# Kernel optimization log

Measured on AMD Instinct MI355X. Metric: run time of the kernel, lower is better.

## Reference

```python
import jax, jax.numpy as jnp
import numpy as np

B, T, N, M = 128, 64, 128, 256


def setup_inputs() -> dict:
    key = jax.random.key(0)
    ks = jax.random.split(key, 8)
    s = 0.05  # small init scale to avoid tanh/sigmoid saturation
    return {
        "data": jax.random.normal(ks[0], (B, T, N), jnp.float32),
        "h0": jnp.zeros((B, M), jnp.float32),
        "c0": jnp.zeros((B, M), jnp.float32),
        "W": jax.random.normal(ks[1], (N, 4 * M), jnp.float32) * s,   # LSTM kernel (i,f,c,o)
        "U": jax.random.normal(ks[2], (M, 4 * M), jnp.float32) * s,   # LSTM recurrent kernel
        "b": jnp.zeros((4 * M,), jnp.float32),
        "w1_k": jax.random.normal(ks[3], (T, T), jnp.float32) * s,
        "w1_b": jnp.zeros((T,), jnp.float32),
        "w2_k": jax.random.normal(ks[4], (2 * M, T), jnp.float32) * s,
        "w2_b": jnp.zeros((T,), jnp.float32),
        "v_k": jax.random.normal(ks[5], (T, 1), jnp.float32) * s,
        "v_b": jnp.zeros((1,), jnp.float32),
        "n": N,
    }


def reference(data, h0, c0, W, U, b, w1_k, w1_b, w2_k, w2_b, v_k, v_b, n):
    Tn = data.shape[1]
    # w1 applied to x_perm = (B, n, T); constant across timesteps -> precompute
    w1x = jnp.einsum('btf,ts->bfs', data, w1_k) + w1_b  # (B, n, T)

    def step(carry, x_t):
        h, c = carry
        # keras LSTM cell, gate order i, f, c(g), o
        z = x_t @ W + h @ U + b                      # (B, 4m)
        i, f, g, o = jnp.split(z, 4, axis=-1)
        i = jax.nn.sigmoid(i)
        f = jax.nn.sigmoid(f)
        g = jnp.tanh(g)
        o = jax.nn.sigmoid(o)
        c2 = f * c + i * g
        h2 = o * jnp.tanh(c2)
        # input attention, computed with post-step (h2, c2) as in the original
        q = jnp.concatenate([h2, c2], axis=-1) @ w2_k + w2_b   # (B, T)
        score = jnp.tanh(w1x + q[:, None, :])                  # (B, n, T)
        s = score @ v_k[:, 0] + v_b[0]                         # (B, n)
        alpha = jax.nn.softmax(s, axis=-1)                     # softmax over features n
        return (h2, c2), alpha

    xs = jnp.swapaxes(data, 0, 1)                    # (T, B, n)
    _, alphas = jax.lax.scan(step, (h0, c0), xs)     # (T, B, n)
    # faithful to tf.reshape(stack(T,B,1,n), (-1, T, n)) in the original
    alpha_seq = alphas.reshape(-1, Tn, n)            # (B, T, n)
    return data * alpha_seq
```

## Files before the change

kernel.cpp:

```cpp
#include <hip/hip_runtime.h>

typedef unsigned short u16;
typedef __attribute__((ext_vector_type(8))) short short8;
typedef __attribute__((ext_vector_type(4))) float f32x4;

#define DEVI static __device__ __forceinline__

DEVI u16 f2bf(float f) {
  union { float f; unsigned u; } v; v.f = f;
  unsigned r = v.u + 0x7FFFu + ((v.u >> 16) & 1u);
  return (u16)(r >> 16);
}

DEVI float bf2f(u16 x) {
  union { unsigned u; float f; } v; v.u = ((unsigned)x) << 16;
  return v.f;
}

DEVI short8 pack8(float4 a, float4 b) {
  short8 v;
  v[0] = (short)f2bf(a.x); v[1] = (short)f2bf(a.y);
  v[2] = (short)f2bf(a.z); v[3] = (short)f2bf(a.w);
  v[4] = (short)f2bf(b.x); v[5] = (short)f2bf(b.y);
  v[6] = (short)f2bf(b.z); v[7] = (short)f2bf(b.w);
  return v;
}

DEVI float sigm(float x) {
  return __builtin_amdgcn_rcpf(1.f + __expf(-x));
}
DEVI float tanh_(float x) {
  return 1.f - 2.f * __builtin_amdgcn_rcpf(__expf(2.f * x) + 1.f);
}

__global__ __launch_bounds__(256) void k_prep(
    const float* __restrict__ W, const float* __restrict__ U,
    const float* __restrict__ w2k, u16* __restrict__ Wt,
    u16* __restrict__ Ut, u16* __restrict__ w2t) {
  int idx = blockIdx.x * 256 + threadIdx.x;
  int stride = gridDim.x * 256;
  for (int i = idx; i < 256 * 1024; i += stride) {
    int k = i >> 10, j = i & 1023;
    Ut[j * 256 + k] = f2bf(U[i]);
  }
  for (int i = idx; i < 128 * 1024; i += stride) {
    int k = i >> 10, j = i & 1023;
    Wt[j * 128 + k] = f2bf(W[i]);
  }
  for (int i = idx; i < 512 * 64; i += stride) {
    int k = i >> 6, s = i & 63;
    w2t[s * 512 + k] = f2bf(w2k[i]);
  }
}

__global__ __launch_bounds__(512) void k_xw(
    const float* __restrict__ data, const float* __restrict__ bias,
    const u16* __restrict__ Wt, u16* __restrict__ XWf) {
  __shared__ u16 Xs[16][136];
  const int tid = threadIdx.x;
  const int lane = tid & 63;
  const int w = tid >> 6;
  const int l15 = lane & 15;
  const int l4 = lane >> 4;
  const int t = blockIdx.x >> 3, bg = blockIdx.x & 7, b0 = bg << 4;

  if (tid < 256) {
    int row = tid >> 4, cb = (tid & 15) * 8;
    const float4* p = reinterpret_cast<const float4*>(
        &data[(size_t)(b0 + row) * 8192 + t * 128 + cb]);
    float4 va = p[0], vb = p[1];
    *reinterpret_cast<short8*>(&Xs[row][cb]) = pack8(va, vb);
  }
  __syncthreads();

  f32x4 acc[8];
#pragma unroll
  for (int ct = 0; ct < 8; ++ct) {
    float bv = bias[w * 128 + ct * 16 + l15];
    acc[ct] = (f32x4){bv, bv, bv, bv};
  }
#pragma unroll
  for (int kk = 0; kk < 4; ++kk) {
    short8 af = *reinterpret_cast<const short8*>(&Xs[l15][kk * 32 + l4 * 8]);
#pragma unroll
    for (int ct = 0; ct < 8; ++ct) {
      const int col = w * 128 + ct * 16 + l15;
      short8 bf =
          *reinterpret_cast<const short8*>(&Wt[col * 128 + kk * 32 + l4 * 8]);
      acc[ct] = __builtin_amdgcn_mfma_f32_16x16x32_bf16(af, bf, acc[ct], 0, 0, 0);
    }
  }
#pragma unroll
  for (int ct = 0; ct < 8; ++ct) {
    const int ft = w * 8 + ct;
    ushort4 v;
    v.x = f2bf(acc[ct][0]); v.y = f2bf(acc[ct][1]);
    v.z = f2bf(acc[ct][2]); v.w = f2bf(acc[ct][3]);
    *reinterpret_cast<ushort4*>(
        &XWf[((size_t)(t * 8 + bg) * 64 + ft) * 256 + lane * 4]) = v;
  }
}

__global__ __launch_bounds__(512, 2) void k_lstm(
    const float* __restrict__ h0, const float* __restrict__ c0,
    const float* __restrict__ w2b, const u16* __restrict__ Ut,
    const u16* __restrict__ w2t, const u16* __restrict__ XWf,
    float* __restrict__ QS) {
  __shared__ u16 Hs[2][16][264];
  __shared__ u16 Cs[2][16][264];

  const int tid = threadIdx.x;
  const int lane = tid & 63;
  const int w = tid >> 6;
  const int l15 = lane & 15;
  const int l4 = lane >> 4;
  const int bg = blockIdx.x;
  const int b0 = bg << 4;

  {
    int row = tid >> 5, hb = (tid & 31) * 8;
    const float4* p =
        reinterpret_cast<const float4*>(&h0[(size_t)(b0 + row) * 256 + hb]);
    float4 a0 = p[0], a1 = p[1];
    *reinterpret_cast<short8*>(&Hs[0][row][hb]) = pack8(a0, a1);
  }

  float creg[2][4];
#pragma unroll
  for (int n = 0; n < 2; ++n)
#pragma unroll
    for (int r = 0; r < 4; ++r)
      creg[n][r] = c0[(size_t)(b0 + l4 * 4 + r) * 256 + w * 32 + n * 16 + l15];

  float w2bv = (w < 4) ? w2b[w * 16 + l15] : 0.f;

  __syncthreads();

  for (int t = 0; t < 64; ++t) {
    const int cur = t & 1, nxt = cur ^ 1;

    f32x4 acc[4][2];
#pragma unroll
    for (int g = 0; g < 4; ++g)
#pragma unroll
      for (int n = 0; n < 2; ++n) {
        const int ft = g * 16 + w * 2 + n;
        ushort4 v = *reinterpret_cast<const ushort4*>(
            &XWf[((size_t)(t * 8 + bg) * 64 + ft) * 256 + lane * 4]);
        acc[g][n] = (f32x4){bf2f(v.x), bf2f(v.y), bf2f(v.z), bf2f(v.w)};
      }

#pragma unroll
    for (int kk = 0; kk < 8; ++kk) {
      short8 af =
          *reinterpret_cast<const short8*>(&Hs[cur][l15][kk * 32 + l4 * 8]);
#pragma unroll
      for (int g = 0; g < 4; ++g)
#pragma unroll
        for (int n = 0; n < 2; ++n) {
          const int col = g * 256 + w * 32 + n * 16 + l15;
          short8 bf = *reinterpret_cast<const short8*>(
              &Ut[(size_t)col * 256 + kk * 32 + l4 * 8]);
          acc[g][n] =
              __builtin_amdgcn_mfma_f32_16x16x32_bf16(af, bf, acc[g][n], 0, 0, 0);
        }
    }

#pragma unroll
    for (int n = 0; n < 2; ++n)
#pragma unroll
      for (int r = 0; r < 4; ++r) {
        float iv = sigm(acc[0][n][r]);
        float fv = sigm(acc[1][n][r]);
        float gv = tanh_(acc[2][n][r]);
        float ov = sigm(acc[3][n][r]);
        float c2 = fv * creg[n][r] + iv * gv;
        creg[n][r] = c2;
        float h2 = ov * tanh_(c2);
        int m = w * 32 + n * 16 + l15;
        int br = l4 * 4 + r;
        Hs[nxt][br][m] = f2bf(h2);
        Cs[nxt][br][m] = f2bf(c2);
      }
    __syncthreads();

    if (w < 4) {
      f32x4 qa = (f32x4){w2bv, w2bv, w2bv, w2bv};
      const int colq = w * 16 + l15;
#pragma unroll
      for (int kk = 0; kk < 16; ++kk) {
        short8 af;
        if (kk < 8)
          af = *reinterpret_cast<const short8*>(
              &Hs[nxt][l15][kk * 32 + l4 * 8]);
        else
          af = *reinterpret_cast<const short8*>(
              &Cs[nxt][l15][(kk - 8) * 32 + l4 * 8]);
        short8 bf = *reinterpret_cast<const short8*>(
            &w2t[colq * 512 + kk * 32 + l4 * 8]);
        qa = __builtin_amdgcn_mfma_f32_16x16x32_bf16(af, bf, qa, 0, 0, 0);
      }
#pragma unroll
      for (int r = 0; r < 4; ++r)
        QS[(size_t)(t * 128 + b0 + l4 * 4 + r) * 64 + w * 16 + l15] = qa[r];
    }
  }
}

__global__ __launch_bounds__(256) void k_attn(
    const float* __restrict__ data, const float* __restrict__ w1k,
    const float* __restrict__ w1b, const float* __restrict__ vk,
    const float* __restrict__ vb, const float* __restrict__ QS,
    float* __restrict__ out) {
  __shared__ float Xs[64][128];
  __shared__ float Wk[64][64];
  __shared__ float w1x[128][67];
  __shared__ float vls[64];
  __shared__ float qls[2][64];
  __shared__ float red[4][2];

  const int tid = threadIdx.x;
  const int b = blockIdx.x >> 1;
  const int half = blockIdx.x & 1;

#pragma unroll
  for (int c = 0; c < 8; ++c) {
    int i = c * 1024 + tid * 4;
    *reinterpret_cast<float4*>(&Xs[0][0] + i) =
        *reinterpret_cast<const float4*>(&data[(size_t)b * 8192 + i]);
  }
#pragma unroll
  for (int c = 0; c < 4; ++c) {
    int i = c * 1024 + tid * 4;
    *reinterpret_cast<float4*>(&Wk[0][0] + i) =
        *reinterpret_cast<const float4*>(&w1k[i]);
  }
  if (tid < 64) vls[tid] = vk[tid];
  __syncthreads();

  const int f = tid & 127;
  const int sh = tid >> 7;
  const int s0 = sh * 32;
  {
    float a[32];
#pragma unroll
    for (int j = 0; j < 32; ++j) a[j] = w1b[s0 + j];
    for (int t = 0; t < 64; ++t) {
      float xv = Xs[t][f];
#pragma unroll
      for (int j = 0; j < 32; ++j) a[j] = __fmaf_rn(xv, Wk[t][s0 + j], a[j]);
    }
#pragma unroll
    for (int j = 0; j < 32; ++j) w1x[f][s0 + j] = a[j];
  }
  __syncthreads();

  const float vbv = vb[0];
  const int wv = tid >> 6;
  const int lane = tid & 63;

  for (int tt = 0; tt < 16; ++tt) {
    if (tid < 128) {
      int which = tid >> 6, s = tid & 63;
      qls[which][s] =
          QS[(size_t)((half * 32 + tt * 2 + which) * 128 + b) * 64 + s];
    }
    __syncthreads();

    float acc = vbv;
#pragma unroll 8
    for (int s = 0; s < 64; ++s)
      acc += tanh_(w1x[f][s] + qls[sh][s]) * vls[s];

    float m = acc;
#pragma unroll
    for (int o = 32; o > 0; o >>= 1) m = fmaxf(m, __shfl_xor(m, o));
    if (lane == 0) red[wv][0] = m;
    __syncthreads();
    m = fmaxf(red[sh * 2][0], red[sh * 2 + 1][0]);
    float e = __expf(acc - m);
    float sum = e;
#pragma unroll
    for (int o = 32; o > 0; o >>= 1) sum += __shfl_xor(sum, o);
    if (lane == 0) red[wv][1] = sum;
    __syncthreads();
    sum = red[sh * 2][1] + red[sh * 2 + 1][1];
    float alpha = e / sum;

    int t = half * 32 + tt * 2 + sh;
    size_t P = (size_t)t * 128 + b;
    out[P * 128 + f] = data[P * 128 + f] * alpha;
    __syncthreads();
  }
}

extern "C" void kernel_launch(void* const* d_in, const int* in_sizes, int n_in,
                              void* d_out, int out_size, void* d_ws,
                              size_t ws_size, hipStream_t stream) {
  (void)in_sizes; (void)n_in; (void)out_size; (void)ws_size;
  const float* data = (const float*)d_in[0];
  const float* h0   = (const float*)d_in[1];
  const float* c0   = (const float*)d_in[2];
  const float* W    = (const float*)d_in[3];
  const float* U    = (const float*)d_in[4];
  const float* bias = (const float*)d_in[5];
  const float* w1k  = (const float*)d_in[6];
  const float* w1b  = (const float*)d_in[7];
  const float* w2k  = (const float*)d_in[8];
  const float* w2b  = (const float*)d_in[9];
  const float* vk   = (const float*)d_in[10];
  const float* vb   = (const float*)d_in[11];
  float* out = (float*)d_out;

  char* ws = (char*)d_ws;
  float* QS = (float*)(ws);
  u16* Ut   = (u16*)(ws + (2u << 20));
  u16* Wt   = (u16*)(ws + (2u << 20) + 524288);
  u16* w2t  = (u16*)(ws + (2u << 20) + 786432);
  u16* XWf  = (u16*)(ws + (3u << 20));

  k_prep<<<512, 256, 0, stream>>>(W, U, w2k, Wt, Ut, w2t);
  k_xw<<<512, 512, 0, stream>>>(data, bias, Wt, XWf);
  k_lstm<<<8, 512, 0, stream>>>(h0, c0, w2b, Ut, w2t, XWf, QS);
  k_attn<<<256, 256, 0, stream>>>(data, w1k, w1b, vk, vb, QS, out);
}
```

Baseline: 671.9 us.

## Software-pipeline U loads and prefetch XW in LSTM recurrence loop

Restructures the recurrent step so Ut fragments are double-buffered in registers and loaded two k-steps ahead of the MFMAs, with the first two k-slices kept resident across timesteps. The next timestep's XW input tile is prefetched into registers during the current step, and the w2 fragments are loaded up front before the attention MFMAs. Also makes the prep kernel write coalesced and packs h/c bf16 conversion into one instruction. This hides global load latency on the serial critical path at the cost of much higher register pressure under a 2-wave occupancy bound.

```diff
diff --git a/kernel.cpp b/kernel.cpp
--- a/kernel.cpp
+++ b/kernel.cpp
@@ -15,6 +15,12 @@
 DEVI float bf2f(u16 x) {
   union { unsigned u; float f; } v; v.u = ((unsigned)x) << 16;
   return v.f;
+}
+
+DEVI unsigned cvt_pk_bf16(float lo, float hi) {
+  unsigned r;
+  asm("v_cvt_pk_bf16_f32 %0, %1, %2" : "=v"(r) : "v"(lo), "v"(hi));
+  return r;
 }
 
 DEVI short8 pack8(float4 a, float4 b) {
@@ -39,17 +45,17 @@
     u16* __restrict__ Ut, u16* __restrict__ w2t) {
   int idx = blockIdx.x * 256 + threadIdx.x;
   int stride = gridDim.x * 256;
-  for (int i = idx; i < 256 * 1024; i += stride) {
-    int k = i >> 10, j = i & 1023;
-    Ut[j * 256 + k] = f2bf(U[i]);
-  }
-  for (int i = idx; i < 128 * 1024; i += stride) {
-    int k = i >> 10, j = i & 1023;
-    Wt[j * 128 + k] = f2bf(W[i]);
-  }
-  for (int i = idx; i < 512 * 64; i += stride) {
-    int k = i >> 6, s = i & 63;
-    w2t[s * 512 + k] = f2bf(w2k[i]);
+  for (int o = idx; o < 256 * 1024; o += stride) {
+    int j = o >> 8, k = o & 255;
+    Ut[o] = f2bf(U[k * 1024 + j]);
+  }
+  for (int o = idx; o < 128 * 1024; o += stride) {
+    int j = o >> 7, k = o & 127;
+    Wt[o] = f2bf(W[k * 1024 + j]);
+  }
+  for (int o = idx; o < 64 * 512; o += stride) {
+    int s = o >> 9, k = o & 511;
+    w2t[o] = f2bf(w2k[k * 64 + s]);
   }
 }
 
@@ -101,6 +107,22 @@
   }
 }
 
+#define LOADU(dst, kk)                                               \
+  _Pragma("unroll") for (int g = 0; g < 4; ++g)                      \
+  _Pragma("unroll") for (int n = 0; n < 2; ++n)                      \
+      dst[g][n] = *reinterpret_cast<const short8*>(                  \
+          &Ut[ubase[g][n] + (kk) * 32]);
+
+#define MFMA8(src, kk)                                               \
+  {                                                                  \
+    short8 af = *reinterpret_cast<const short8*>(                    \
+        &Hs[cur][l15][(kk) * 32 + l4 * 8]);                          \
+    _Pragma("unroll") for (int g = 0; g < 4; ++g)                    \
+    _Pragma("unroll") for (int n = 0; n < 2; ++n)                    \
+        acc[g][n] = __builtin_amdgcn_mfma_f32_16x16x32_bf16(         \
+            af, src[g][n], acc[g][n], 0, 0, 0);                      \
+  }
+
 __global__ __launch_bounds__(512, 2) void k_lstm(
     const float* __restrict__ h0, const float* __restrict__ c0,
     const float* __restrict__ w2b, const u16* __restrict__ Ut,
@@ -132,39 +154,79 @@
     for (int r = 0; r < 4; ++r)
       creg[n][r] = c0[(size_t)(b0 + l4 * 4 + r) * 256 + w * 32 + n * 16 + l15];
 
-  float w2bv = (w < 4) ? w2b[w * 16 + l15] : 0.f;
+  const float w2bv = (w < 4) ? w2b[w * 16 + l15] : 0.f;
+
+  int ubase[4][2];
+#pragma unroll
+  for (int g = 0; g < 4; ++g)
+#pragma unroll
+    for (int n = 0; n < 2; ++n)
+      ubase[g][n] = (g * 256 + w * 32 + n * 16 + l15) * 256 + l4 * 8;
+
+  short8 up[2][4][2];
+#pragma unroll
+  for (int kk = 0; kk < 2; ++kk)
+#pragma unroll
+    for (int g = 0; g < 4; ++g)
+#pragma unroll
+      for (int n = 0; n < 2; ++n)
+        up[kk][g][n] =
+            *reinterpret_cast<const short8*>(&Ut[ubase[g][n] + kk * 32]);
+
+  int xoff[4][2];
+#pragma unroll
+  for (int g = 0; g < 4; ++g)
+#pragma unroll
+    for (int n = 0; n < 2; ++n)
+      xoff[g][n] = (bg * 64 + g * 16 + w * 2 + n) * 256 + lane * 4;
+  ushort4 xwb[4][2];
+#pragma unroll
+  for (int g = 0; g < 4; ++g)
+#pragma unroll
+    for (int n = 0; n < 2; ++n)
+      xwb[g][n] = *reinterpret_cast<const ushort4*>(&XWf[xoff[g][n]]);
+
+  int wqoff = (w * 16 + l15) * 512 + l4 * 8;
 
   __syncthreads();
 
   for (int t = 0; t < 64; ++t) {
     const int cur = t & 1, nxt = cur ^ 1;
 
+#pragma unroll
+    for (int g = 0; g < 4; ++g)
+#pragma unroll
+      for (int n = 0; n < 2; ++n) asm("" : "+v"(ubase[g][n]));
+    asm("" : "+v"(wqoff));
+
     f32x4 acc[4][2];
 #pragma unroll
     for (int g = 0; g < 4; ++g)
 #pragma unroll
-      for (int n = 0; n < 2; ++n) {
-        const int ft = g * 16 + w * 2 + n;
-        ushort4 v = *reinterpret_cast<const ushort4*>(
-            &XWf[((size_t)(t * 8 + bg) * 64 + ft) * 256 + lane * 4]);
-        acc[g][n] = (f32x4){bf2f(v.x), bf2f(v.y), bf2f(v.z), bf2f(v.w)};
-      }
-
-#pragma unroll
-    for (int kk = 0; kk < 8; ++kk) {
-      short8 af =
-          *reinterpret_cast<const short8*>(&Hs[cur][l15][kk * 32 + l4 * 8]);
+      for (int n = 0; n < 2; ++n)
+        acc[g][n] = (f32x4){bf2f(xwb[g][n].x), bf2f(xwb[g][n].y),
+                            bf2f(xwb[g][n].z), bf2f(xwb[g][n].w)};
+
+    if (t < 63) {
 #pragma unroll
       for (int g = 0; g < 4; ++g)
 #pragma unroll
-        for (int n = 0; n < 2; ++n) {
-          const int col = g * 256 + w * 32 + n * 16 + l15;
-          short8 bf = *reinterpret_cast<const short8*>(
-              &Ut[(size_t)col * 256 + kk * 32 + l4 * 8]);
-          acc[g][n] =
-              __builtin_amdgcn_mfma_f32_16x16x32_bf16(af, bf, acc[g][n], 0, 0, 0);
-        }
-    }
+        for (int n = 0; n < 2; ++n)
+          xwb[g][n] = *reinterpret_cast<const ushort4*>(
+              &XWf[(t + 1) * 131072 + xoff[g][n]]);
+    }
+
+    short8 sA[4][2], sB[4][2];
+    LOADU(sA, 2);
+    LOADU(sB, 3);
+    MFMA8(up[0], 0);
+    MFMA8(up[1], 1);
+    MFMA8(sA, 2); LOADU(sA, 4);
+    MFMA8(sB, 3); LOADU(sB, 5);
+    MFMA8(sA, 4); LOADU(sA, 6);
+    MFMA8(sB, 5); LOADU(sB, 7);
+    MFMA8(sA, 6);
+    MFMA8(sB, 7);
 
 #pragma unroll
     for (int n = 0; n < 2; ++n)
@@ -177,16 +239,21 @@
         float c2 = fv * creg[n][r] + iv * gv;
         creg[n][r] = c2;
         float h2 = ov * tanh_(c2);
+        unsigned pk = cvt_pk_bf16(h2, c2);
         int m = w * 32 + n * 16 + l15;
         int br = l4 * 4 + r;
-        Hs[nxt][br][m] = f2bf(h2);
-        Cs[nxt][br][m] = f2bf(c2);
+        Hs[nxt][br][m] = (u16)pk;
+        Cs[nxt][br][m] = (u16)(pk >> 16);
       }
+
     __syncthreads();
 
     if (w < 4) {
+      short8 wq[16];
+#pragma unroll
+      for (int kk = 0; kk < 16; ++kk)
+        wq[kk] = *reinterpret_cast<const short8*>(&w2t[wqoff + kk * 32]);
       f32x4 qa = (f32x4){w2bv, w2bv, w2bv, w2bv};
-      const int colq = w * 16 + l15;
 #pragma unroll
       for (int kk = 0; kk < 16; ++kk) {
         short8 af;
@@ -196,9 +263,7 @@
         else
           af = *reinterpret_cast<const short8*>(
               &Cs[nxt][l15][(kk - 8) * 32 + l4 * 8]);
-        short8 bf = *reinterpret_cast<const short8*>(
-            &w2t[colq * 512 + kk * 32 + l4 * 8]);
-        qa = __builtin_amdgcn_mfma_f32_16x16x32_bf16(af, bf, qa, 0, 0, 0);
+        qa = __builtin_amdgcn_mfma_f32_16x16x32_bf16(af, wq[kk], qa, 0, 0, 0);
       }
 #pragma unroll
       for (int r = 0; r < 4; ++r)
```

Result: slower. 1.028 ms (+53.0%).

## Fuse input projection into LSTM kernel with 1024-thread blocks and prefetched x_t

Applied to the files above, without the earlier changes.

Removes the separate k_xw kernel and its bf16 XWf intermediate. The LSTM kernel now computes x_t@W + h@U in a single 12-step MFMA loop per timestep. The block grows to 1024 threads (16 waves), so each wave owns 16 hidden columns instead of 32, which halves the per-wave MFMA chain on the serial critical path. Waves 4-7 prefetch and convert the next timestep's data into shared memory while waves 0-3 compute the attention query. This costs an extra barrier per step and more W reads from global/L2 inside the recurrent loop, and the w1x padding in k_attn changes.

```diff
diff --git a/kernel.cpp b/kernel.cpp
--- a/kernel.cpp
+++ b/kernel.cpp
@@ -10,11 +10,6 @@
   union { float f; unsigned u; } v; v.f = f;
   unsigned r = v.u + 0x7FFFu + ((v.u >> 16) & 1u);
   return (u16)(r >> 16);
-}
-
-DEVI float bf2f(u16 x) {
-  union { unsigned u; float f; } v; v.u = ((unsigned)x) << 16;
-  return v.f;
 }
 
 DEVI short8 pack8(float4 a, float4 b) {
@@ -53,135 +48,97 @@
   }
 }
 
-__global__ __launch_bounds__(512) void k_xw(
-    const float* __restrict__ data, const float* __restrict__ bias,
-    const u16* __restrict__ Wt, u16* __restrict__ XWf) {
+__global__ __launch_bounds__(1024, 4) void k_lstm(
+    const float* __restrict__ data, const float* __restrict__ h0,
+    const float* __restrict__ c0, const float* __restrict__ bias,
+    const float* __restrict__ w2b, const u16* __restrict__ Wt,
+    const u16* __restrict__ Ut, const u16* __restrict__ w2t,
+    float* __restrict__ QS) {
   __shared__ u16 Xs[16][136];
+  __shared__ u16 Hs[2][16][264];
+  __shared__ u16 Cs[16][264];
+
   const int tid = threadIdx.x;
   const int lane = tid & 63;
   const int w = tid >> 6;
   const int l15 = lane & 15;
   const int l4 = lane >> 4;
-  const int t = blockIdx.x >> 3, bg = blockIdx.x & 7, b0 = bg << 4;
+  const int b0 = blockIdx.x << 4;
 
   if (tid < 256) {
     int row = tid >> 4, cb = (tid & 15) * 8;
-    const float4* p = reinterpret_cast<const float4*>(
-        &data[(size_t)(b0 + row) * 8192 + t * 128 + cb]);
-    float4 va = p[0], vb = p[1];
-    *reinterpret_cast<short8*>(&Xs[row][cb]) = pack8(va, vb);
-  }
-  __syncthreads();
-
-  f32x4 acc[8];
-#pragma unroll
-  for (int ct = 0; ct < 8; ++ct) {
-    float bv = bias[w * 128 + ct * 16 + l15];
-    acc[ct] = (f32x4){bv, bv, bv, bv};
-  }
-#pragma unroll
-  for (int kk = 0; kk < 4; ++kk) {
-    short8 af = *reinterpret_cast<const short8*>(&Xs[l15][kk * 32 + l4 * 8]);
-#pragma unroll
-    for (int ct = 0; ct < 8; ++ct) {
-      const int col = w * 128 + ct * 16 + l15;
-      short8 bf =
-          *reinterpret_cast<const short8*>(&Wt[col * 128 + kk * 32 + l4 * 8]);
-      acc[ct] = __builtin_amdgcn_mfma_f32_16x16x32_bf16(af, bf, acc[ct], 0, 0, 0);
-    }
-  }
-#pragma unroll
-  for (int ct = 0; ct < 8; ++ct) {
-    const int ft = w * 8 + ct;
-    ushort4 v;
-    v.x = f2bf(acc[ct][0]); v.y = f2bf(acc[ct][1]);
-    v.z = f2bf(acc[ct][2]); v.w = f2bf(acc[ct][3]);
-    *reinterpret_cast<ushort4*>(
-        &XWf[((size_t)(t * 8 + bg) * 64 + ft) * 256 + lane * 4]) = v;
-  }
-}
-
-__global__ __launch_bounds__(512, 2) void k_lstm(
-    const float* __restrict__ h0, const float* __restrict__ c0,
-    const float* __restrict__ w2b, const u16* __restrict__ Ut,
-    const u16* __restrict__ w2t, const u16* __restrict__ XWf,
-    float* __restrict__ QS) {
-  __shared__ u16 Hs[2][16][264];
-  __shared__ u16 Cs[2][16][264];
-
-  const int tid = threadIdx.x;
-  const int lane = tid & 63;
-  const int w = tid >> 6;
-  const int l15 = lane & 15;
-  const int l4 = lane >> 4;
-  const int bg = blockIdx.x;
-  const int b0 = bg << 4;
-
-  {
-    int row = tid >> 5, hb = (tid & 31) * 8;
+    const float4* p =
+        reinterpret_cast<const float4*>(&data[(size_t)(b0 + row) * 8192 + cb]);
+    float4 a = p[0], b = p[1];
+    *reinterpret_cast<short8*>(&Xs[row][cb]) = pack8(a, b);
+  } else if (tid < 512) {
+    int t2 = tid - 256;
+    int row = t2 >> 4, hb = (t2 & 15) * 16;
     const float4* p =
         reinterpret_cast<const float4*>(&h0[(size_t)(b0 + row) * 256 + hb]);
-    float4 a0 = p[0], a1 = p[1];
+    float4 a0 = p[0], a1 = p[1], a2 = p[2], a3 = p[3];
     *reinterpret_cast<short8*>(&Hs[0][row][hb]) = pack8(a0, a1);
-  }
-
-  float creg[2][4];
-#pragma unroll
-  for (int n = 0; n < 2; ++n)
-#pragma unroll
-    for (int r = 0; r < 4; ++r)
-      creg[n][r] = c0[(size_t)(b0 + l4 * 4 + r) * 256 + w * 32 + n * 16 + l15];
-
-  float w2bv = (w < 4) ? w2b[w * 16 + l15] : 0.f;
+    *reinterpret_cast<short8*>(&Hs[0][row][hb + 8]) = pack8(a2, a3);
+  }
+
+  float creg[4];
+#pragma unroll
+  for (int r = 0; r < 4; ++r)
+    creg[r] = c0[(size_t)(b0 + l4 * 4 + r) * 256 + w * 16 + l15];
+
+  float bz[4];
+#pragma unroll
+  for (int g = 0; g < 4; ++g) bz[g] = bias[g * 256 + w * 16 + l15];
+
+  const float w2bv = (w < 4) ? w2b[w * 16 + l15] : 0.f;
 
   __syncthreads();
 
   for (int t = 0; t < 64; ++t) {
     const int cur = t & 1, nxt = cur ^ 1;
 
-    f32x4 acc[4][2];
+    f32x4 acc[4];
 #pragma unroll
     for (int g = 0; g < 4; ++g)
-#pragma unroll
-      for (int n = 0; n < 2; ++n) {
-        const int ft = g * 16 + w * 2 + n;
-        ushort4 v = *reinterpret_cast<const ushort4*>(
-            &XWf[((size_t)(t * 8 + bg) * 64 + ft) * 256 + lane * 4]);
-        acc[g][n] = (f32x4){bf2f(v.x), bf2f(v.y), bf2f(v.z), bf2f(v.w)};
+      acc[g] = (f32x4){bz[g], bz[g], bz[g], bz[g]};
+
+#pragma unroll
+    for (int kk = 0; kk < 12; ++kk) {
+      short8 af;
+      if (kk < 4)
+        af = *reinterpret_cast<const short8*>(&Xs[l15][kk * 32 + l4 * 8]);
+      else
+        af = *reinterpret_cast<const short8*>(
+            &Hs[cur][l15][(kk - 4) * 32 + l4 * 8]);
+#pragma unroll
+      for (int g = 0; g < 4; ++g) {
+        const int col = g * 256 + w * 16 + l15;
+        short8 bf;
+        if (kk < 4)
+          bf = *reinterpret_cast<const short8*>(
+              &Wt[col * 128 + kk * 32 + l4 * 8]);
+        else
+          bf = *reinterpret_cast<const short8*>(
+              &Ut[(size_t)col * 256 + (kk - 4) * 32 + l4 * 8]);
+        acc[g] =
+            __builtin_amdgcn_mfma_f32_16x16x32_bf16(af, bf, acc[g], 0, 0, 0);
       }
-
-#pragma unroll
-    for (int kk = 0; kk < 8; ++kk) {
-      short8 af =
-          *reinterpret_cast<const short8*>(&Hs[cur][l15][kk * 32 + l4 * 8]);
-#pragma unroll
-      for (int g = 0; g < 4; ++g)
-#pragma unroll
-        for (int n = 0; n < 2; ++n) {
-          const int col = g * 256 + w * 32 + n * 16 + l15;
-          short8 bf = *reinterpret_cast<const short8*>(
-              &Ut[(size_t)col * 256 + kk * 32 + l4 * 8]);
-          acc[g][n] =
-              __builtin_amdgcn_mfma_f32_16x16x32_bf16(af, bf, acc[g][n], 0, 0, 0);
-        }
-    }
-
-#pragma unroll
-    for (int n = 0; n < 2; ++n)
-#pragma unroll
-      for (int r = 0; r < 4; ++r) {
-        float iv = sigm(acc[0][n][r]);
-        float fv = sigm(acc[1][n][r]);
-        float gv = tanh_(acc[2][n][r]);
-        float ov = sigm(acc[3][n][r]);
-        float c2 = fv * creg[n][r] + iv * gv;
-        creg[n][r] = c2;
-        float h2 = ov * tanh_(c2);
-        int m = w * 32 + n * 16 + l15;
-        int br = l4 * 4 + r;
-        Hs[nxt][br][m] = f2bf(h2);
-        Cs[nxt][br][m] = f2bf(c2);
-      }
+    }
+
+#pragma unroll
+    for (int r = 0; r < 4; ++r) {
+      float iv = sigm(acc[0][r]);
+      float fv = sigm(acc[1][r]);
+      float gv = tanh_(acc[2][r]);
+      float ov = sigm(acc[3][r]);
+      float c2 = fv * creg[r] + iv * gv;
+      creg[r] = c2;
+      float h2 = ov * tanh_(c2);
+      int m = w * 16 + l15;
+      int br = l4 * 4 + r;
+      Hs[nxt][br][m] = f2bf(h2);
+      Cs[br][m] = f2bf(c2);
+    }
     __syncthreads();
 
     if (w < 4) {
@@ -195,7 +152,7 @@
               &Hs[nxt][l15][kk * 32 + l4 * 8]);
         else
           af = *reinterpret_cast<const short8*>(
-              &Cs[nxt][l15][(kk - 8) * 32 + l4 * 8]);
+              &Cs[l15][(kk - 8) * 32 + l4 * 8]);
         short8 bf = *reinterpret_cast<const short8*>(
             &w2t[colq * 512 + kk * 32 + l4 * 8]);
         qa = __builtin_amdgcn_mfma_f32_16x16x32_bf16(af, bf, qa, 0, 0, 0);
@@ -203,7 +160,15 @@
 #pragma unroll
       for (int r = 0; r < 4; ++r)
         QS[(size_t)(t * 128 + b0 + l4 * 4 + r) * 64 + w * 16 + l15] = qa[r];
-    }
+    } else if (w < 8 && t < 63) {
+      int t2 = tid - 256;
+      int row = t2 >> 4, cb = (t2 & 15) * 8;
+      const float4* p = reinterpret_cast<const float4*>(
+          &data[(size_t)(b0 + row) * 8192 + (t + 1) * 128 + cb]);
+      float4 a = p[0], b = p[1];
+      *reinterpret_cast<short8*>(&Xs[row][cb]) = pack8(a, b);
+    }
+    __syncthreads();
   }
 }
 
@@ -214,7 +179,7 @@
     float* __restrict__ out) {
   __shared__ float Xs[64][128];
   __shared__ float Wk[64][64];
-  __shared__ float w1x[128][67];
+  __shared__ float w1x[128][66];
   __shared__ float vls[64];
   __shared__ float qls[2][64];
   __shared__ float red[4][2];
@@ -313,14 +278,12 @@
   float* out = (float*)d_out;
 
   char* ws = (char*)d_ws;
-  float* QS = (float*)(ws);
-  u16* Ut   = (u16*)(ws + (2u << 20));
-  u16* Wt   = (u16*)(ws + (2u << 20) + 524288);
-  u16* w2t  = (u16*)(ws + (2u << 20) + 786432);
-  u16* XWf  = (u16*)(ws + (3u << 20));
+  u16* Ut   = (u16*)(ws);
+  u16* Wt   = (u16*)(ws + 524288);
+  u16* w2t  = (u16*)(ws + 786432);
+  float* QS = (float*)(ws + 851968);
 
   k_prep<<<512, 256, 0, stream>>>(W, U, w2k, Wt, Ut, w2t);
-  k_xw<<<512, 512, 0, stream>>>(data, bias, Wt, XWf);
-  k_lstm<<<8, 512, 0, stream>>>(h0, c0, w2b, Ut, w2t, XWf, QS);
+  k_lstm<<<8, 1024, 0, stream>>>(data, h0, c0, bias, w2b, Wt, Ut, w2t, QS);
   k_attn<<<256, 256, 0, stream>>>(data, w1k, w1b, vk, vb, QS, out);
 }
```

New measurement: 1.227 ms. 1.83x slower.
